# Kernel optimization log

Hardware: AMD Instinct MI355X
Metric: run time of the kernel (lower is better)

## Reference

```python
import jax, jax.numpy as jnp
import numpy as np

N_NODES = 100000
N_EDGES = 1600000


def _tconv(x, src, dst, Wq, bq, Wk, bk, Wv, bv, Ws, bs):
    """PyG TransformerConv (heads=1, concat=True, root_weight=True), eval mode."""
    n = x.shape[0]
    q = x @ Wq + bq          # [N, d]
    k = x @ Wk + bk
    v = x @ Wv + bv
    scale = 1.0 / jnp.sqrt(jnp.asarray(q.shape[1], q.dtype))
    # per-edge attention logits: query at destination, key at source
    alpha = jnp.sum(q[dst] * k[src], axis=-1) * scale       # [E]
    # segment softmax over incoming edges of each destination node
    m = jax.ops.segment_max(alpha, dst, num_segments=n)      # [N]
    e = jnp.exp(alpha - m[dst])
    s = jax.ops.segment_sum(e, dst, num_segments=n)          # [N]
    a = e / s[dst]                                           # [E]
    agg = jax.ops.segment_sum(a[:, None] * v[src], dst, num_segments=n)  # [N, d]
    return agg + x @ Ws + bs  # skip connection (root_weight=True)


def setup_inputs() -> dict:
    key = jax.random.key(0)
    ks = jax.random.split(key, 20)
    x = jax.random.normal(ks[0], (N_NODES, 2), dtype=jnp.float32)
    edge_index = jax.random.randint(ks[1], (2, N_EDGES), 0, N_NODES, dtype=jnp.int64)
    def lin(k, din, dout):
        k1, k2 = jax.random.split(k)
        lim = 1.0 / np.sqrt(din)
        W = jax.random.uniform(k1, (din, dout), jnp.float32, -lim, lim)
        b = jax.random.uniform(k2, (dout,), jnp.float32, -lim, lim)
        return W, b
    Wq1, bq1 = lin(ks[2], 2, 256)
    Wk1, bk1 = lin(ks[3], 2, 256)
    Wv1, bv1 = lin(ks[4], 2, 256)
    Ws1, bs1 = lin(ks[5], 2, 256)
    Wq2, bq2 = lin(ks[6], 256, 2)
    Wk2, bk2 = lin(ks[7], 256, 2)
    Wv2, bv2 = lin(ks[8], 256, 2)
    Ws2, bs2 = lin(ks[9], 256, 2)
    return dict(x=x, edge_index=edge_index,
                Wq1=Wq1, bq1=bq1, Wk1=Wk1, bk1=bk1, Wv1=Wv1, bv1=bv1, Ws1=Ws1, bs1=bs1,
                Wq2=Wq2, bq2=bq2, Wk2=Wk2, bk2=bk2, Wv2=Wv2, bv2=bv2, Ws2=Ws2, bs2=bs2)


def reference(x, edge_index,
              Wq1, bq1, Wk1, bk1, Wv1, bv1, Ws1, bs1,
              Wq2, bq2, Wk2, bk2, Wv2, bv2, Ws2, bs2):
    src, dst = edge_index[0], edge_index[1]
    h = _tconv(x, src, dst, Wq1, bq1, Wk1, bk1, Wv1, bv1, Ws1, bs1)
    h = jax.nn.relu(h)
    # F.dropout is identity in eval mode
    h = _tconv(h, src, dst, Wq2, bq2, Wk2, bk2, Wv2, bv2, Ws2, bs2)
    return jax.nn.log_softmax(h, axis=1)
```

## Files before the change

### kernel.cpp

```cpp
#include <hip/hip_runtime.h>


#define R_LOG2   8
#define R_DSTS   256
#define BE       4096
#define MAXNB    512
#define CAPB     4608
#define S_SLICES 4
#define RSQRT2   0.70710678118654752f

__global__ __launch_bounds__(1024) void scatter1_k(
        const int* __restrict__ src, const int* __restrict__ dst,
        int* __restrict__ cnt, int* __restrict__ recs, int NB, int E) {
    __shared__ int hist[MAXNB];
    __shared__ int lofs[MAXNB];
    __shared__ int gbase[MAXNB];
    __shared__ int stage[BE];
    __shared__ unsigned short sbkt[BE];
    __shared__ int wsum[16];
    int t = threadIdx.x;
    if (t < NB) hist[t] = 0;
    __syncthreads();

    int base = blockIdx.x * BE;
    int nloc = E - base; if (nloc > BE) nloc = BE;
    int nv = nloc >> 2;
    const int4* d4 = (const int4*)(dst + base);
    const int4* s4 = (const int4*)(src + base);

    for (int i = t; i < nv; i += 1024) {
        int4 v = d4[i];
        atomicAdd(&hist[v.x >> R_LOG2], 1);
        atomicAdd(&hist[v.y >> R_LOG2], 1);
        atomicAdd(&hist[v.z >> R_LOG2], 1);
        atomicAdd(&hist[v.w >> R_LOG2], 1);
    }
    for (int i = (nv << 2) + t; i < nloc; i += 1024)
        atomicAdd(&hist[dst[base + i] >> R_LOG2], 1);
    __syncthreads();

    {
        int v = (t < NB) ? hist[t] : 0;
        int lane = t & 63, w = t >> 6;
        int incl = v;
#pragma unroll
        for (int o = 1; o < 64; o <<= 1) {
            int u = __shfl_up(incl, o);
            if (lane >= o) incl += u;
        }
        if (lane == 63) wsum[w] = incl;
        __syncthreads();
        int ex = incl - v;
        for (int j = 0; j < w; ++j) ex += wsum[j];
        if (t < NB) lofs[t] = ex;
    }
    __syncthreads();

    if (t < NB) {
        int h = hist[t];
        int start = h ? atomicAdd(&cnt[t], h) : 0;
        gbase[t] = t * CAPB + start - lofs[t];
        hist[t] = 0;
    }
    __syncthreads();

    for (int i = t; i < nv; i += 1024) {
        int4 dv = d4[i];
        int4 sv = s4[i];
        int d, b, r, p;
        d = dv.x; b = d >> R_LOG2; r = atomicAdd(&hist[b], 1); p = lofs[b] + r;
        stage[p] = sv.x | ((d & (R_DSTS - 1)) << 17); sbkt[p] = (unsigned short)b;
        d = dv.y; b = d >> R_LOG2; r = atomicAdd(&hist[b], 1); p = lofs[b] + r;
        stage[p] = sv.y | ((d & (R_DSTS - 1)) << 17); sbkt[p] = (unsigned short)b;
        d = dv.z; b = d >> R_LOG2; r = atomicAdd(&hist[b], 1); p = lofs[b] + r;
        stage[p] = sv.z | ((d & (R_DSTS - 1)) << 17); sbkt[p] = (unsigned short)b;
        d = dv.w; b = d >> R_LOG2; r = atomicAdd(&hist[b], 1); p = lofs[b] + r;
        stage[p] = sv.w | ((d & (R_DSTS - 1)) << 17); sbkt[p] = (unsigned short)b;
    }
    for (int i = (nv << 2) + t; i < nloc; i += 1024) {
        int d = dst[base + i];
        int b = d >> R_LOG2;
        int r = atomicAdd(&hist[b], 1);
        int p = lofs[b] + r;
        stage[p] = src[base + i] | ((d & (R_DSTS - 1)) << 17);
        sbkt[p] = (unsigned short)b;
    }
    __syncthreads();

    for (int i = t; i < nloc; i += 1024) {
        int bk = sbkt[i];
        int p = gbase[bk] + i;
        if (p < (bk + 1) * CAPB) recs[p] = stage[i];
    }
}

__global__ __launch_bounds__(256) void l1r_k(
        const float* __restrict__ x,
        const float* __restrict__ Wq1, const float* __restrict__ bq1,
        const float* __restrict__ Wk1, const float* __restrict__ bk1,
        const int* __restrict__ recs, const int* __restrict__ cnt,
        float* __restrict__ part, int N) {
    __shared__ float p0[R_DSTS], p1[R_DSTS], pc[R_DSTS];
    __shared__ float ac[3 * R_DSTS];
    __shared__ float cpart[4][9];
    __shared__ float c9[9];
    int t = threadIdx.x;

    {
        float wq0 = Wq1[t], wq1 = Wq1[256 + t];
        float wk0 = Wk1[t], wk1 = Wk1[256 + t];
        float bq = bq1[t], bk = bk1[t];
        float vals[9] = { wq0 * wk0, wq0 * wk1, wq1 * wk0, wq1 * wk1,
                          wq0 * bk,  wq1 * bk,  bq * wk0,  bq * wk1,  bq * bk };
        int lane = t & 63, w = t >> 6;
#pragma unroll
        for (int i = 0; i < 9; ++i) {
            float v = vals[i];
#pragma unroll
            for (int o = 32; o > 0; o >>= 1) v += __shfl_xor(v, o);
            if (lane == 0) cpart[w][i] = v;
        }
        __syncthreads();
        if (t < 9) c9[t] = cpart[0][t] + cpart[1][t] + cpart[2][t] + cpart[3][t];
        __syncthreads();
    }

    int bs = blockIdx.x;
    int b = bs >> 2;
    int sl = bs & 3;
    int nbase = b << R_LOG2;
    int rem = N - nbase; if (rem > R_DSTS) rem = R_DSTS;

    ac[t] = 0.f; ac[256 + t] = 0.f; ac[512 + t] = 0.f;
    if (t < rem) {
        float2 xd = ((const float2*)x)[nbase + t];
        p0[t] = c9[0] * xd.x + c9[2] * xd.y + c9[6];
        p1[t] = c9[1] * xd.x + c9[3] * xd.y + c9[7];
        pc[t] = c9[4] * xd.x + c9[5] * xd.y + c9[8];
    }
    __syncthreads();

    int cb = cnt[b]; if (cb > CAPB) cb = CAPB;
    int len = (cb + S_SLICES - 1) / S_SLICES;
    int lo = sl * len;
    int hi = lo + len; if (hi > cb) hi = cb;
    const int* rb = recs + (size_t)b * CAPB;
    for (int i = lo + t; i < hi; i += 256) {
        int rec = rb[i];
        int s = rec & 0x1FFFF;
        int dl = (rec >> 17) & (R_DSTS - 1);
        float2 xs = ((const float2*)x)[s];
        float w = __expf((p0[dl] * xs.x + p1[dl] * xs.y + pc[dl]) * 0.0625f);
        atomicAdd(&ac[dl], w);
        atomicAdd(&ac[256 + dl], w * xs.x);
        atomicAdd(&ac[512 + dl], w * xs.y);
    }
    __syncthreads();

    float* dp = part + (size_t)bs * (3 * R_DSTS);
    dp[t] = ac[t];
    dp[256 + t] = ac[256 + t];
    dp[512 + t] = ac[512 + t];
}

__global__ __launch_bounds__(256, 4) void proj_k(
        const float* __restrict__ x, const float* __restrict__ part,
        const float* __restrict__ Wv1, const float* __restrict__ bv1,
        const float* __restrict__ Ws1, const float* __restrict__ bs1,
        const float* __restrict__ Wq2, const float* __restrict__ bq2,
        const float* __restrict__ Wk2, const float* __restrict__ bk2,
        const float* __restrict__ Wv2, const float* __restrict__ bv2,
        const float* __restrict__ Ws2, const float* __restrict__ bs2,
        float* __restrict__ q2, float4* __restrict__ kv2,
        float* __restrict__ hs2, int N) {
    __shared__ float sW[14][256];
    int t = threadIdx.x;
    sW[0][t]  = Wv1[t];
    sW[1][t]  = Wv1[256 + t];
    sW[2][t]  = Ws1[t];
    sW[3][t]  = Ws1[256 + t];
    sW[4][t]  = bv1[t];
    sW[5][t]  = bs1[t];
    sW[6][t]  = Wq2[2 * t];
    sW[7][t]  = Wq2[2 * t + 1];
    sW[8][t]  = Wk2[2 * t];
    sW[9][t]  = Wk2[2 * t + 1];
    sW[10][t] = Wv2[2 * t];
    sW[11][t] = Wv2[2 * t + 1];
    sW[12][t] = Ws2[2 * t];
    sW[13][t] = Ws2[2 * t + 1];
    __syncthreads();

    int g = t & 7;
    int grp = t >> 3;
    int nb = blockIdx.x * 64 + grp * 2;

    float a0[2], a1[2], he[2], xdx[2], xdy[2];
#pragma unroll
    for (int k = 0; k < 2; ++k) {
        int n = nb + k;
        float s = 0.f, sx0 = 0.f, sx1 = 0.f;
        if (n < N) {
            int b = n >> R_LOG2, idx = n & (R_DSTS - 1);
            const float* pp = part + ((size_t)(b * S_SLICES + (g & 3))) * (3 * R_DSTS) + idx;
            s = pp[0]; sx0 = pp[256]; sx1 = pp[512];
        }
#pragma unroll
        for (int m = 1; m < 4; m <<= 1) {
            s   += __shfl_xor(s, m);
            sx0 += __shfl_xor(sx0, m);
            sx1 += __shfl_xor(sx1, m);
        }
        a0[k] = 0.f; a1[k] = 0.f; he[k] = 0.f;
        if (s > 0.f) {
            float inv = 1.0f / s;
            a0[k] = sx0 * inv; a1[k] = sx1 * inv; he[k] = 1.f;
        }
        float2 xd = make_float2(0.f, 0.f);
        if (n < N) xd = ((const float2*)x)[n];
        xdx[k] = xd.x; xdy[k] = xd.y;
    }

    float acc[2][8];
#pragma unroll
    for (int k = 0; k < 2; ++k)
#pragma unroll
        for (int i = 0; i < 8; ++i) acc[k][i] = 0.f;

#pragma unroll 1
    for (int j = 0; j < 8; ++j) {
        int ci = g + 8 * j;
        float4 hk[2];
        {
            float4 w0 = ((const float4*)sW[0])[ci];
            float4 w1 = ((const float4*)sW[1])[ci];
            float4 w2 = ((const float4*)sW[2])[ci];
            float4 w3 = ((const float4*)sW[3])[ci];
            float4 w4 = ((const float4*)sW[4])[ci];
            float4 w5 = ((const float4*)sW[5])[ci];
#pragma unroll
            for (int k = 0; k < 2; ++k) {
                hk[k].x = fmaxf(a0[k]*w0.x + a1[k]*w1.x + xdx[k]*w2.x + xdy[k]*w3.x + he[k]*w4.x + w5.x, 0.f);
                hk[k].y = fmaxf(a0[k]*w0.y + a1[k]*w1.y + xdx[k]*w2.y + xdy[k]*w3.y + he[k]*w4.y + w5.y, 0.f);
                hk[k].z = fmaxf(a0[k]*w0.z + a1[k]*w1.z + xdx[k]*w2.z + xdy[k]*w3.z + he[k]*w4.z + w5.z, 0.f);
                hk[k].w = fmaxf(a0[k]*w0.w + a1[k]*w1.w + xdx[k]*w2.w + xdy[k]*w3.w + he[k]*w4.w + w5.w, 0.f);
            }
        }
#pragma unroll
        for (int i = 0; i < 8; ++i) {
            float4 u = ((const float4*)sW[6 + i])[ci];
#pragma unroll
            for (int k = 0; k < 2; ++k)
                acc[k][i] += hk[k].x*u.x + hk[k].y*u.y + hk[k].z*u.z + hk[k].w*u.w;
        }
    }
#pragma unroll
    for (int k = 0; k < 2; ++k)
#pragma unroll
        for (int i = 0; i < 8; ++i) {
#pragma unroll
            for (int m = 1; m < 8; m <<= 1)
                acc[k][i] += __shfl_xor(acc[k][i], m);
        }
    if (g < 2) {
        int n = nb + g;
        if (n < N) {
            ((float2*)q2)[n]  = make_float2(acc[g][0] + bq2[0], acc[g][1] + bq2[1]);
            kv2[n] = make_float4(acc[g][2] + bk2[0], acc[g][3] + bk2[1],
                                 acc[g][4] + bv2[0], acc[g][5] + bv2[1]);
            ((float2*)hs2)[n] = make_float2(acc[g][6] + bs2[0], acc[g][7] + bs2[1]);
        }
    }
}

__global__ __launch_bounds__(256) void l2r_k(
        const float* __restrict__ q2, const float4* __restrict__ kv2,
        const int* __restrict__ recs, const int* __restrict__ cnt,
        float* __restrict__ part, int N) {
    __shared__ float qx[R_DSTS], qy[R_DSTS];
    __shared__ float ac[3 * R_DSTS];
    int t = threadIdx.x;
    int bs = blockIdx.x;
    int b = bs >> 2;
    int sl = bs & 3;
    int nbase = b << R_LOG2;
    int rem = N - nbase; if (rem > R_DSTS) rem = R_DSTS;

    ac[t] = 0.f; ac[256 + t] = 0.f; ac[512 + t] = 0.f;
    if (t < rem) {
        float2 q = ((const float2*)q2)[nbase + t];
        qx[t] = q.x * RSQRT2;
        qy[t] = q.y * RSQRT2;
    }
    __syncthreads();

    int cb = cnt[b]; if (cb > CAPB) cb = CAPB;
    int len = (cb + S_SLICES - 1) / S_SLICES;
    int lo = sl * len;
    int hi = lo + len; if (hi > cb) hi = cb;
    const int* rb = recs + (size_t)b * CAPB;
    for (int i = lo + t; i < hi; i += 256) {
        int rec = rb[i];
        int s = rec & 0x1FFFF;
        int dl = (rec >> 17) & (R_DSTS - 1);
        float4 kv = kv2[s];
        float w = __expf(qx[dl] * kv.x + qy[dl] * kv.y);
        atomicAdd(&ac[dl], w);
        atomicAdd(&ac[256 + dl], w * kv.z);
        atomicAdd(&ac[512 + dl], w * kv.w);
    }
    __syncthreads();

    float* dp = part + (size_t)bs * (3 * R_DSTS);
    dp[t] = ac[t];
    dp[256 + t] = ac[256 + t];
    dp[512 + t] = ac[512 + t];
}

__global__ __launch_bounds__(256) void out2x_k(
        const float* __restrict__ part, const float* __restrict__ hs2,
        float* __restrict__ out, int N) {
    int t = threadIdx.x;
    int g = t & 7;
    int n = blockIdx.x * 32 + (t >> 3);
    if (n >= N) return;
    int b = n >> R_LOG2, idx = n & (R_DSTS - 1);

    const float* pp = part + ((size_t)(b * S_SLICES + (g & 3))) * (3 * R_DSTS) + idx;
    float s = pp[0], sv0 = pp[256], sv1 = pp[512];
#pragma unroll
    for (int m = 1; m < 4; m <<= 1) {
        s   += __shfl_xor(s, m);
        sv0 += __shfl_xor(sv0, m);
        sv1 += __shfl_xor(sv1, m);
    }
    if (g != 0) return;

    float g0 = 0.f, g1 = 0.f;
    if (s > 0.f) {
        float inv = 1.0f / s;
        g0 = sv0 * inv; g1 = sv1 * inv;
    }
    float2 hs = ((const float2*)hs2)[n];
    float o0 = g0 + hs.x;
    float o1 = g1 + hs.y;
    float mx = fmaxf(o0, o1), mn = fminf(o0, o1);
    float lse = mx + log1pf(__expf(mn - mx));
    ((float2*)out)[n] = make_float2(o0 - lse, o1 - lse);
}

extern "C" void kernel_launch(void* const* d_in, const int* in_sizes, int n_in,
                              void* d_out, int out_size, void* d_ws, size_t ws_size,
                              hipStream_t stream) {
    const float* x   = (const float*)d_in[0];
    const int*   ei  = (const int*)d_in[1];
    const float* Wq1 = (const float*)d_in[2];
    const float* bq1 = (const float*)d_in[3];
    const float* Wk1 = (const float*)d_in[4];
    const float* bk1 = (const float*)d_in[5];
    const float* Wv1 = (const float*)d_in[6];
    const float* bv1 = (const float*)d_in[7];
    const float* Ws1 = (const float*)d_in[8];
    const float* bs1 = (const float*)d_in[9];
    const float* Wq2 = (const float*)d_in[10];
    const float* bq2 = (const float*)d_in[11];
    const float* Wk2 = (const float*)d_in[12];
    const float* bk2 = (const float*)d_in[13];
    const float* Wv2 = (const float*)d_in[14];
    const float* bv2 = (const float*)d_in[15];
    const float* Ws2 = (const float*)d_in[16];
    const float* bs2 = (const float*)d_in[17];

    const int N = in_sizes[0] / 2;
    const int E = in_sizes[1] / 2;
    const int* src = ei;
    const int* dst = ei + E;

    const int NB   = (N + R_DSTS - 1) >> R_LOG2;
    const int NBlk = (E + BE - 1) / BE;

    float* ws = (float*)d_ws;
    size_t off = 0;
    int*   cnt   = (int*)(ws + off);         off += NB;
    int*   recs  = (int*)(ws + off);         off += (size_t)NB * CAPB;
    off = (off + 3) & ~(size_t)3;
    float* part  = ws + off;                 off += (size_t)NB * S_SLICES * 3 * R_DSTS;
    float4* kv2  = (float4*)(ws + off);      off += 4 * (size_t)N;
    float* q2    = ws + off;                 off += 2 * (size_t)N;
    float* hs2   = ws + off;                 off += 2 * (size_t)N;

    const int gP  = (N + 63) / 64;
    const int gO  = (N + 31) / 32;

    hipMemsetAsync(cnt, 0, NB * sizeof(int), stream);
    scatter1_k<<<NBlk, 1024, 0, stream>>>(src, dst, cnt, recs, NB, E);
    l1r_k<<<NB * S_SLICES, 256, 0, stream>>>(x, Wq1, bq1, Wk1, bk1,
                                             recs, cnt, part, N);
    proj_k<<<gP, 256, 0, stream>>>(x, part, Wv1, bv1, Ws1, bs1,
                                   Wq2, bq2, Wk2, bk2, Wv2, bv2, Ws2, bs2,
                                   q2, kv2, hs2, N);
    l2r_k<<<NB * S_SLICES, 256, 0, stream>>>(q2, kv2, recs, cnt, part, N);
    out2x_k<<<gO, 256, 0, stream>>>(part, hs2, (float*)d_out, N);
}
```

Before: 123.0 us.

## Replace sliced partial aggregation with one 1024-thread block per bucket

Each destination bucket's edge records are now aggregated by a single 1024-thread block instead of four 256-thread slice blocks. Per-slice partials no longer go to global memory and get combined later. The layer-2 aggregation now also does the final normalize, skip-add and log-softmax, which removes the separate out2x kernel launch and the partial buffer traffic. In exchange the grid shrinks to about 391 blocks, which may leave parts of the GPU idle, and shared-memory atomics within each block become more contended.

New measurement: 123.4 us. Within noise of the previous version (+0.3%).

```diff
diff --git a/kernel.cpp b/kernel.cpp
--- a/kernel.cpp
+++ b/kernel.cpp
@@ -6,7 +6,6 @@
 #define BE       4096
 #define MAXNB    512
 #define CAPB     4608
-#define S_SLICES 4
 #define RSQRT2   0.70710678118654752f
 
 __global__ __launch_bounds__(1024) void scatter1_k(
@@ -94,19 +93,19 @@
     }
 }
 
-__global__ __launch_bounds__(256) void l1r_k(
+__global__ __launch_bounds__(1024) void l1agg_k(
         const float* __restrict__ x,
         const float* __restrict__ Wq1, const float* __restrict__ bq1,
         const float* __restrict__ Wk1, const float* __restrict__ bk1,
         const int* __restrict__ recs, const int* __restrict__ cnt,
-        float* __restrict__ part, int N) {
+        float4* __restrict__ agg1, int N) {
+    __shared__ float cpart[4][9];
+    __shared__ float c9[9];
     __shared__ float p0[R_DSTS], p1[R_DSTS], pc[R_DSTS];
     __shared__ float ac[3 * R_DSTS];
-    __shared__ float cpart[4][9];
-    __shared__ float c9[9];
     int t = threadIdx.x;
 
-    {
+    if (t < 256) {
         float wq0 = Wq1[t], wq1 = Wq1[256 + t];
         float wk0 = Wk1[t], wk1 = Wk1[256 + t];
         float bq = bq1[t], bk = bk1[t];
@@ -120,32 +119,29 @@
             for (int o = 32; o > 0; o >>= 1) v += __shfl_xor(v, o);
             if (lane == 0) cpart[w][i] = v;
         }
-        __syncthreads();
-        if (t < 9) c9[t] = cpart[0][t] + cpart[1][t] + cpart[2][t] + cpart[3][t];
-        __syncthreads();
-    }
-
-    int bs = blockIdx.x;
-    int b = bs >> 2;
-    int sl = bs & 3;
+    }
+    __syncthreads();
+    if (t < 9) c9[t] = cpart[0][t] + cpart[1][t] + cpart[2][t] + cpart[3][t];
+    __syncthreads();
+
+    int b = blockIdx.x;
     int nbase = b << R_LOG2;
     int rem = N - nbase; if (rem > R_DSTS) rem = R_DSTS;
 
-    ac[t] = 0.f; ac[256 + t] = 0.f; ac[512 + t] = 0.f;
-    if (t < rem) {
-        float2 xd = ((const float2*)x)[nbase + t];
-        p0[t] = c9[0] * xd.x + c9[2] * xd.y + c9[6];
-        p1[t] = c9[1] * xd.x + c9[3] * xd.y + c9[7];
-        pc[t] = c9[4] * xd.x + c9[5] * xd.y + c9[8];
+    if (t < 256) {
+        ac[t] = 0.f; ac[256 + t] = 0.f; ac[512 + t] = 0.f;
+        if (t < rem) {
+            float2 xd = ((const float2*)x)[nbase + t];
+            p0[t] = c9[0] * xd.x + c9[2] * xd.y + c9[6];
+            p1[t] = c9[1] * xd.x + c9[3] * xd.y + c9[7];
+            pc[t] = c9[4] * xd.x + c9[5] * xd.y + c9[8];
+        }
     }
     __syncthreads();
 
     int cb = cnt[b]; if (cb > CAPB) cb = CAPB;
-    int len = (cb + S_SLICES - 1) / S_SLICES;
-    int lo = sl * len;
-    int hi = lo + len; if (hi > cb) hi = cb;
     const int* rb = recs + (size_t)b * CAPB;
-    for (int i = lo + t; i < hi; i += 256) {
+    for (int i = t; i < cb; i += 1024) {
         int rec = rb[i];
         int s = rec & 0x1FFFF;
         int dl = (rec >> 17) & (R_DSTS - 1);
@@ -157,14 +153,12 @@
     }
     __syncthreads();
 
-    float* dp = part + (size_t)bs * (3 * R_DSTS);
-    dp[t] = ac[t];
-    dp[256 + t] = ac[256 + t];
-    dp[512 + t] = ac[512 + t];
+    if (t < rem)
+        agg1[nbase + t] = make_float4(ac[t], ac[256 + t], ac[512 + t], 0.f);
 }
 
 __global__ __launch_bounds__(256, 4) void proj_k(
-        const float* __restrict__ x, const float* __restrict__ part,
+        const float* __restrict__ x, const float4* __restrict__ agg1,
         const float* __restrict__ Wv1, const float* __restrict__ bv1,
         const float* __restrict__ Ws1, const float* __restrict__ bs1,
         const float* __restrict__ Wq2, const float* __restrict__ bq2,
@@ -199,26 +193,16 @@
 #pragma unroll
     for (int k = 0; k < 2; ++k) {
         int n = nb + k;
-        float s = 0.f, sx0 = 0.f, sx1 = 0.f;
+        a0[k] = 0.f; a1[k] = 0.f; he[k] = 0.f; xdx[k] = 0.f; xdy[k] = 0.f;
         if (n < N) {
-            int b = n >> R_LOG2, idx = n & (R_DSTS - 1);
-            const float* pp = part + ((size_t)(b * S_SLICES + (g & 3))) * (3 * R_DSTS) + idx;
-            s = pp[0]; sx0 = pp[256]; sx1 = pp[512];
-        }
-#pragma unroll
-        for (int m = 1; m < 4; m <<= 1) {
-            s   += __shfl_xor(s, m);
-            sx0 += __shfl_xor(sx0, m);
-            sx1 += __shfl_xor(sx1, m);
-        }
-        a0[k] = 0.f; a1[k] = 0.f; he[k] = 0.f;
-        if (s > 0.f) {
-            float inv = 1.0f / s;
-            a0[k] = sx0 * inv; a1[k] = sx1 * inv; he[k] = 1.f;
-        }
-        float2 xd = make_float2(0.f, 0.f);
-        if (n < N) xd = ((const float2*)x)[n];
-        xdx[k] = xd.x; xdy[k] = xd.y;
+            float4 ag = agg1[n];
+            if (ag.x > 0.f) {
+                float inv = 1.0f / ag.x;
+                a0[k] = ag.y * inv; a1[k] = ag.z * inv; he[k] = 1.f;
+            }
+            float2 xd = ((const float2*)x)[n];
+            xdx[k] = xd.x; xdy[k] = xd.y;
+        }
     }
 
     float acc[2][8];
@@ -273,33 +257,31 @@
     }
 }
 
-__global__ __launch_bounds__(256) void l2r_k(
+__global__ __launch_bounds__(1024) void l2out_k(
         const float* __restrict__ q2, const float4* __restrict__ kv2,
+        const float* __restrict__ hs2,
         const int* __restrict__ recs, const int* __restrict__ cnt,
-        float* __restrict__ part, int N) {
+        float* __restrict__ out, int N) {
     __shared__ float qx[R_DSTS], qy[R_DSTS];
     __shared__ float ac[3 * R_DSTS];
     int t = threadIdx.x;
-    int bs = blockIdx.x;
-    int b = bs >> 2;
-    int sl = bs & 3;
+    int b = blockIdx.x;
     int nbase = b << R_LOG2;
     int rem = N - nbase; if (rem > R_DSTS) rem = R_DSTS;
 
-    ac[t] = 0.f; ac[256 + t] = 0.f; ac[512 + t] = 0.f;
-    if (t < rem) {
-        float2 q = ((const float2*)q2)[nbase + t];
-        qx[t] = q.x * RSQRT2;
-        qy[t] = q.y * RSQRT2;
+    if (t < 256) {
+        ac[t] = 0.f; ac[256 + t] = 0.f; ac[512 + t] = 0.f;
+        if (t < rem) {
+            float2 q = ((const float2*)q2)[nbase + t];
+            qx[t] = q.x * RSQRT2;
+            qy[t] = q.y * RSQRT2;
+        }
     }
     __syncthreads();
 
     int cb = cnt[b]; if (cb > CAPB) cb = CAPB;
-    int len = (cb + S_SLICES - 1) / S_SLICES;
-    int lo = sl * len;
-    int hi = lo + len; if (hi > cb) hi = cb;
     const int* rb = recs + (size_t)b * CAPB;
-    for (int i = lo + t; i < hi; i += 256) {
+    for (int i = t; i < cb; i += 1024) {
         int rec = rb[i];
         int s = rec & 0x1FFFF;
         int dl = (rec >> 17) & (R_DSTS - 1);
@@ -311,42 +293,21 @@
     }
     __syncthreads();
 
-    float* dp = part + (size_t)bs * (3 * R_DSTS);
-    dp[t] = ac[t];
-    dp[256 + t] = ac[256 + t];
-    dp[512 + t] = ac[512 + t];
-}
-
-__global__ __launch_bounds__(256) void out2x_k(
-        const float* __restrict__ part, const float* __restrict__ hs2,
-        float* __restrict__ out, int N) {
-    int t = threadIdx.x;
-    int g = t & 7;
-    int n = blockIdx.x * 32 + (t >> 3);
-    if (n >= N) return;
-    int b = n >> R_LOG2, idx = n & (R_DSTS - 1);
-
-    const float* pp = part + ((size_t)(b * S_SLICES + (g & 3))) * (3 * R_DSTS) + idx;
-    float s = pp[0], sv0 = pp[256], sv1 = pp[512];
-#pragma unroll
-    for (int m = 1; m < 4; m <<= 1) {
-        s   += __shfl_xor(s, m);
-        sv0 += __shfl_xor(sv0, m);
-        sv1 += __shfl_xor(sv1, m);
-    }
-    if (g != 0) return;
-
-    float g0 = 0.f, g1 = 0.f;
-    if (s > 0.f) {
-        float inv = 1.0f / s;
-        g0 = sv0 * inv; g1 = sv1 * inv;
-    }
-    float2 hs = ((const float2*)hs2)[n];
-    float o0 = g0 + hs.x;
-    float o1 = g1 + hs.y;
-    float mx = fmaxf(o0, o1), mn = fminf(o0, o1);
-    float lse = mx + log1pf(__expf(mn - mx));
-    ((float2*)out)[n] = make_float2(o0 - lse, o1 - lse);
+    if (t < rem) {
+        int n = nbase + t;
+        float s = ac[t];
+        float g0 = 0.f, g1 = 0.f;
+        if (s > 0.f) {
+            float inv = 1.0f / s;
+            g0 = ac[256 + t] * inv; g1 = ac[512 + t] * inv;
+        }
+        float2 hs = ((const float2*)hs2)[n];
+        float o0 = g0 + hs.x;
+        float o1 = g1 + hs.y;
+        float mx = fmaxf(o0, o1), mn = fminf(o0, o1);
+        float lse = mx + log1pf(__expf(mn - mx));
+        ((float2*)out)[n] = make_float2(o0 - lse, o1 - lse);
+    }
 }
 
 extern "C" void kernel_launch(void* const* d_in, const int* in_sizes, int n_in,
@@ -384,21 +345,18 @@
     int*   cnt   = (int*)(ws + off);         off += NB;
     int*   recs  = (int*)(ws + off);         off += (size_t)NB * CAPB;
     off = (off + 3) & ~(size_t)3;
-    float* part  = ws + off;                 off += (size_t)NB * S_SLICES * 3 * R_DSTS;
+    float4* agg1 = (float4*)(ws + off);      off += 4 * (size_t)N;
     float4* kv2  = (float4*)(ws + off);      off += 4 * (size_t)N;
     float* q2    = ws + off;                 off += 2 * (size_t)N;
     float* hs2   = ws + off;                 off += 2 * (size_t)N;
 
-    const int gP  = (N + 63) / 64;
-    const int gO  = (N + 31) / 32;
+    const int gP = (N + 63) / 64;
 
     hipMemsetAsync(cnt, 0, NB * sizeof(int), stream);
     scatter1_k<<<NBlk, 1024, 0, stream>>>(src, dst, cnt, recs, NB, E);
-    l1r_k<<<NB * S_SLICES, 256, 0, stream>>>(x, Wq1, bq1, Wk1, bk1,
-                                             recs, cnt, part, N);
-    proj_k<<<gP, 256, 0, stream>>>(x, part, Wv1, bv1, Ws1, bs1,
+    l1agg_k<<<NB, 1024, 0, stream>>>(x, Wq1, bq1, Wk1, bk1, recs, cnt, agg1, N);
+    proj_k<<<gP, 256, 0, stream>>>(x, agg1, Wv1, bv1, Ws1, bs1,
                                    Wq2, bq2, Wk2, bk2, Wv2, bv2, Ws2, bs2,
                                    q2, kv2, hs2, N);
-    l2r_k<<<NB * S_SLICES, 256, 0, stream>>>(q2, kv2, recs, cnt, part, N);
-    out2x_k<<<gO, 256, 0, stream>>>(part, hs2, (float*)d_out, N);
-}
+    l2out_k<<<NB, 1024, 0, stream>>>(q2, kv2, hs2, recs, cnt, (float*)d_out, N);
+}
```
